# Kernel optimization log

Hardware: AMD Instinct MI355X
Metric: run time of the kernel (lower is better)

Reference implementation:

```python
import jax, jax.numpy as jnp
import numpy as np

D = 1024      # features
C = 768       # context dim
H = 16        # heads
HD = D // H   # head dim = 64
N = 2048      # query tokens
M = 2048      # context tokens
EPS = 1e-12
SCALE = float(np.sqrt(HD))


def layernorm(x, w, b):
    c = x - x.mean(axis=-1, keepdims=True)
    s = (c * c).mean(axis=-1, keepdims=True)
    return c * jax.lax.rsqrt(s + EPS) * w + b


def setup_inputs() -> dict:
    key = jax.random.key(0)
    ks = jax.random.split(key, 10)
    sc = 0.02
    return {
        "x": jax.random.normal(ks[0], (N, D), jnp.float32),
        "ctx": jax.random.normal(ks[1], (M, C), jnp.float32),
        # attention projections (Projection: normal*0.02, zero bias)
        "wq": jax.random.normal(ks[2], (D, D), jnp.float32) * sc,
        "bq": jnp.zeros((D,), jnp.float32),
        "wk": jax.random.normal(ks[3], (C, D), jnp.float32) * sc,
        "bk": jnp.zeros((D,), jnp.float32),
        "wv": jax.random.normal(ks[4], (C, D), jnp.float32) * sc,
        "bv": jnp.zeros((D,), jnp.float32),
        "wo": jax.random.normal(ks[5], (D, D), jnp.float32) * sc,
        "bo": jnp.zeros((D,), jnp.float32),
        # MLP
        "w1": jax.random.normal(ks[6], (D, 4 * D), jnp.float32) * sc,
        "b1": jnp.zeros((4 * D,), jnp.float32),
        "w2": jax.random.normal(ks[7], (4 * D, D), jnp.float32) * sc,
        "b2": jnp.zeros((D,), jnp.float32),
        # layernorms
        "qn_w": jnp.ones((D,), jnp.float32), "qn_b": jnp.zeros((D,), jnp.float32),
        "kvn_w": jnp.ones((C,), jnp.float32), "kvn_b": jnp.zeros((C,), jnp.float32),
        "pn_w": jnp.ones((D,), jnp.float32), "pn_b": jnp.zeros((D,), jnp.float32),
    }


def reference(x, ctx, wq, bq, wk, bk, wv, bv, wo, bo, w1, b1, w2, b2,
              qn_w, qn_b, kvn_w, kvn_b, pn_w, pn_b):
    # pre-norm cross-attention
    xq = layernorm(x, qn_w, qn_b)          # [n, d]
    kv = layernorm(ctx, kvn_w, kvn_b)      # [m, c]
    q = (xq @ wq + bq).reshape(N, H, HD).transpose(1, 0, 2)   # [h, n, hd]
    k = (kv @ wk + bk).reshape(M, H, HD).transpose(1, 0, 2)   # [h, m, hd]
    v = (kv @ wv + bv).reshape(M, H, HD).transpose(1, 0, 2)   # [h, m, hd]
    attn = jax.nn.softmax(jnp.einsum('hnd,hmd->hnm', q, k) / SCALE, axis=-1)
    o = jnp.einsum('hnm,hmd->hnd', attn, v).transpose(1, 0, 2).reshape(N, D)
    x = (o @ wo + bo) + x
    # MLP block
    h = layernorm(x, pn_w, pn_b)
    h = jax.nn.gelu(h @ w1 + b1) @ w2 + b2
    return h + x
```

## Files before the change

### kernel.cpp

```cpp
#include <hip/hip_runtime.h>

typedef __bf16 bf16;
typedef __bf16 bf16x4 __attribute__((ext_vector_type(4)));
typedef __bf16 bf16x8 __attribute__((ext_vector_type(8)));
typedef float f32x4 __attribute__((ext_vector_type(4)));

#define N_TOK 2048
#define M_TOK 2048
#define DIM 1024
#define CDIM 768
#define DFF 4096

static __device__ __forceinline__ void async16(const void* g, void* l) {
  __builtin_amdgcn_global_load_lds((const __attribute__((address_space(1))) void*)g,
                                   (__attribute__((address_space(3))) void*)l, 16, 0, 0);
}

__global__ __launch_bounds__(256) void detect_kernel(const void* x, int* flag) {
  __shared__ int cnt;
  if (threadIdx.x == 0) cnt = 0;
  __syncthreads();
  const unsigned* w = (const unsigned*)x;
  int ok = 0;
  for (int i = threadIdx.x; i < 512; i += 256) {
    unsigned lo = w[i] & 0xFFFFu;
    float f = __uint_as_float(lo << 16);
    if (lo == 0u || (fabsf(f) > 1e-3f && fabsf(f) < 1e3f)) ok++;
  }
  atomicAdd(&cnt, ok);
  __syncthreads();
  if (threadIdx.x == 0) *flag = (cnt >= 256) ? 1 : 0;
}

struct ConvArgs {
  const void* src[12];
  bf16* dst[12];
  int n[12];
};
__global__ __launch_bounds__(256) void conv_small_kernel(ConvArgs a, const int* flag) {
  const bool isbf = (*flag != 0);
  const int b = blockIdx.x;
  const void* in = a.src[b];
  bf16* out = a.dst[b];
  const int n = a.n[b];
  for (int i = threadIdx.x; i < n; i += 256)
    out[i] = isbf ? ((const bf16*)in)[i] : (bf16)((const float*)in)[i];
}

struct TmArgs {
  const void* src[4];
  bf16* dst[4];
  int r0[4], Rcnt[4], c0[4], Cfull[4], gx[4], gy[4];
  int force_bf;
};
__global__ __launch_bounds__(256) void tmulti_kernel(TmArgs a, const int* flag) {
  const int z = blockIdx.z;
  if ((int)blockIdx.x >= a.gx[z] || (int)blockIdx.y >= a.gy[z]) return;
  __shared__ bf16 t[32][33];
  const bool isbf = a.force_bf || (*flag != 0);
  const void* in = a.src[z];
  bf16* out = a.dst[z];
  const int Rcnt = a.Rcnt[z], Cfull = a.Cfull[z];
  const int cb = blockIdx.x * 32, rb = blockIdx.y * 32;
  const int tx = threadIdx.x & 31, ty = threadIdx.x >> 5;
#pragma unroll
  for (int i = 0; i < 4; i++) {
    const size_t r = (size_t)(a.r0[z] + rb + ty + i * 8);
    const size_t c = (size_t)(a.c0[z] + cb + tx);
    float v = isbf ? (float)((const bf16*)in)[r * Cfull + c]
                   : ((const float*)in)[r * Cfull + c];
    t[ty + i * 8][tx] = (bf16)v;
  }
  __syncthreads();
#pragma unroll
  for (int i = 0; i < 4; i++)
    out[(size_t)(cb + ty + i * 8) * Rcnt + rb + tx] = t[tx][ty + i * 8];
}

__global__ __launch_bounds__(256) void ln_pair_kernel(
    const void* __restrict__ x0, const bf16* w0, const bf16* b0, bf16* o0,
    const void* __restrict__ x1, const bf16* w1, const bf16* b1, bf16* o1,
    const int* flag) {
  const bool isbf = (*flag != 0);
  const int cols = (blockIdx.y == 0) ? DIM : CDIM;
  const void* x = (blockIdx.y == 0) ? x0 : x1;
  const bf16* w = (blockIdx.y == 0) ? w0 : w1;
  const bf16* b = (blockIdx.y == 0) ? b0 : b1;
  bf16* outp = (blockIdx.y == 0) ? o0 : o1;
  const int row = blockIdx.x;
  const bf16* xr_b = (const bf16*)x + (size_t)row * cols;
  const float* xr_f = (const float*)x + (size_t)row * cols;
  bf16* orow = outp + (size_t)row * cols;
  float s = 0.f, ss = 0.f;
  for (int c = threadIdx.x; c < cols; c += 256) {
    float v = isbf ? (float)xr_b[c] : xr_f[c];
    s += v; ss += v * v;
  }
  for (int d = 1; d < 64; d <<= 1) { s += __shfl_xor(s, d, 64); ss += __shfl_xor(ss, d, 64); }
  __shared__ float sh[8];
  const int wv = threadIdx.x >> 6, lane = threadIdx.x & 63;
  if (lane == 0) { sh[wv] = s; sh[4 + wv] = ss; }
  __syncthreads();
  s = sh[0] + sh[1] + sh[2] + sh[3];
  ss = sh[4] + sh[5] + sh[6] + sh[7];
  const float mean = s / cols;
  float var = ss / cols - mean * mean;
  var = fmaxf(var, 0.f);
  const float r = rsqrtf(var + 1e-12f);
  for (int c = threadIdx.x; c < cols; c += 256) {
    float v = isbf ? (float)xr_b[c] : xr_f[c];
    orow[c] = (bf16)((v - mean) * r * (float)w[c] + (float)b[c]);
  }
}

__global__ __launch_bounds__(256) void ln_kernel(
    const bf16* __restrict__ x, const bf16* __restrict__ w, const bf16* __restrict__ b,
    bf16* __restrict__ out, int cols) {
  const int row = blockIdx.x;
  const bf16* xr = x + (size_t)row * cols;
  bf16* orow = out + (size_t)row * cols;
  float s = 0.f, ss = 0.f;
  for (int c = threadIdx.x; c < cols; c += 256) {
    float v = (float)xr[c];
    s += v; ss += v * v;
  }
  for (int d = 1; d < 64; d <<= 1) { s += __shfl_xor(s, d, 64); ss += __shfl_xor(ss, d, 64); }
  __shared__ float sh[8];
  const int wv = threadIdx.x >> 6, lane = threadIdx.x & 63;
  if (lane == 0) { sh[wv] = s; sh[4 + wv] = ss; }
  __syncthreads();
  s = sh[0] + sh[1] + sh[2] + sh[3];
  ss = sh[4] + sh[5] + sh[6] + sh[7];
  const float mean = s / cols;
  float var = ss / cols - mean * mean;
  var = fmaxf(var, 0.f);
  const float r = rsqrtf(var + 1e-12f);
  for (int c = threadIdx.x; c < cols; c += 256) {
    float v = (float)xr[c];
    orow[c] = (bf16)((v - mean) * r * (float)w[c] + (float)b[c]);
  }
}

__device__ __forceinline__ float gelu_f(float x) {
  float u = 0.7978845608028654f * (x + 0.044715f * x * x * x);
  return 0.5f * x * (1.f + tanhf(u));
}

template <int EPI>
__global__ __launch_bounds__(256) void gemm64(
    const bf16* __restrict__ A, const bf16* __restrict__ Bt,
    const bf16* __restrict__ bias, const void* __restrict__ resid,
    void* __restrict__ Cout, int K, int ldc, const int* flag) {
  __shared__ __align__(16) bf16 As[64 * 32];
  __shared__ __align__(16) bf16 Bs[64 * 32];
  const int tid = threadIdx.x;
  const int lane = tid & 63, wv = tid >> 6;
  const int lq = lane >> 4, lm = lane & 15;
  const int row0 = blockIdx.y * 64, col0 = blockIdx.x * 64;
  const int wr = (wv >> 1) * 32, wc = (wv & 1) * 32;

  f32x4 acc[2][2] = {};
  const int r_a = wv * 16 + (lane >> 2);
  const int kc = (lane & 3) * 8;

  for (int k0 = 0; k0 < K; k0 += 32) {
    __syncthreads();
    async16(A + (size_t)(row0 + r_a) * K + k0 + kc, As + wv * 512);
    async16(Bt + (size_t)(col0 + r_a) * K + k0 + kc, Bs + wv * 512);
    __syncthreads();
    bf16x8 af[2], bfv[2];
#pragma unroll
    for (int t = 0; t < 2; t++) af[t] = *(const bf16x8*)&As[(wr + t * 16 + lm) * 32 + lq * 8];
#pragma unroll
    for (int t = 0; t < 2; t++) bfv[t] = *(const bf16x8*)&Bs[(wc + t * 16 + lm) * 32 + lq * 8];
#pragma unroll
    for (int i = 0; i < 2; i++)
#pragma unroll
      for (int j = 0; j < 2; j++)
        acc[i][j] = __builtin_amdgcn_mfma_f32_16x16x32_bf16(af[i], bfv[j], acc[i][j], 0, 0, 0);
  }

  const bool isbf = (*flag != 0);
#pragma unroll
  for (int i = 0; i < 2; i++) {
    const int rb = row0 + wr + i * 16 + lq * 4;
#pragma unroll
    for (int j = 0; j < 2; j++) {
      const int c = col0 + wc + j * 16 + lm;
      const float bv = (EPI != 5) ? (float)bias[c] : 0.f;
#pragma unroll
      for (int rg = 0; rg < 4; rg++) {
        const size_t idx = (size_t)(rb + rg) * ldc + c;
        float v = acc[i][j][rg] + bv;
        if (EPI == 1)
          v += isbf ? (float)((const bf16*)resid)[idx] : ((const float*)resid)[idx];
        if (EPI == 2) v = gelu_f(v);
        if (EPI == 4) v += (float)((const bf16*)resid)[idx];
        if (EPI == 5)
          v += isbf ? (float)((bf16*)Cout)[idx] : ((float*)Cout)[idx];
        if (EPI == 4 || EPI == 5) {
          if (isbf) ((bf16*)Cout)[idx] = (bf16)v;
          else      ((float*)Cout)[idx] = v;
        } else {
          ((bf16*)Cout)[idx] = (bf16)v;
        }
      }
    }
  }
}

struct QkvArgs {
  const bf16* A[3];
  const bf16* Bt[3];
  const bf16* bias[3];
  bf16* C[3];
  int K[3];
};
__global__ __launch_bounds__(256) void gemm64_qkv(QkvArgs a) {
  const int z = blockIdx.z;
  const bf16* A = a.A[z];
  const bf16* Bt = a.Bt[z];
  const int K = a.K[z];
  __shared__ __align__(16) bf16 As[64 * 32];
  __shared__ __align__(16) bf16 Bs[64 * 32];
  const int tid = threadIdx.x;
  const int lane = tid & 63, wv = tid >> 6;
  const int lq = lane >> 4, lm = lane & 15;
  const int row0 = blockIdx.y * 64, col0 = blockIdx.x * 64;
  const int wr = (wv >> 1) * 32, wc = (wv & 1) * 32;

  f32x4 acc[2][2] = {};
  const int r_a = wv * 16 + (lane >> 2);
  const int kc = (lane & 3) * 8;

  for (int k0 = 0; k0 < K; k0 += 32) {
    __syncthreads();
    async16(A + (size_t)(row0 + r_a) * K + k0 + kc, As + wv * 512);
    async16(Bt + (size_t)(col0 + r_a) * K + k0 + kc, Bs + wv * 512);
    __syncthreads();
    bf16x8 af[2], bfv[2];
#pragma unroll
    for (int t = 0; t < 2; t++) af[t] = *(const bf16x8*)&As[(wr + t * 16 + lm) * 32 + lq * 8];
#pragma unroll
    for (int t = 0; t < 2; t++) bfv[t] = *(const bf16x8*)&Bs[(wc + t * 16 + lm) * 32 + lq * 8];
#pragma unroll
    for (int i = 0; i < 2; i++)
#pragma unroll
      for (int j = 0; j < 2; j++)
        acc[i][j] = __builtin_amdgcn_mfma_f32_16x16x32_bf16(af[i], bfv[j], acc[i][j], 0, 0, 0);
  }

  const bf16* bias = a.bias[z];
  bf16* C = a.C[z];
#pragma unroll
  for (int i = 0; i < 2; i++) {
    const int rb = row0 + wr + i * 16 + lq * 4;
#pragma unroll
    for (int j = 0; j < 2; j++) {
      const int c = col0 + wc + j * 16 + lm;
      const float bv = (float)bias[c];
#pragma unroll
      for (int rg = 0; rg < 4; rg++)
        C[(size_t)(rb + rg) * DIM + c] = (bf16)(acc[i][j][rg] + bv);
    }
  }
}

#define KS_STR 72
#define VS_STR 136
__global__ __launch_bounds__(256) void attn_kernel(
    const bf16* __restrict__ q, const bf16* __restrict__ k,
    const bf16* __restrict__ vT, bf16* __restrict__ o) {
  __shared__ __align__(16) bf16 Ks[128 * KS_STR];
  __shared__ __align__(16) bf16 Vs[64 * VS_STR];
  __shared__ __align__(16) bf16 Ps[64 * VS_STR];
  const int tid = threadIdx.x, lane = tid & 63, wv = tid >> 6;
  const int lq = lane >> 4, lm = lane & 15;
  const int h = blockIdx.y;
  const int n0 = blockIdx.x * 64;

  bf16x8 qf[2];
#pragma unroll
  for (int f = 0; f < 2; f++)
    qf[f] = *(const bf16x8*)&q[(size_t)(n0 + wv * 16 + lm) * DIM + h * 64 + f * 32 + lq * 8];

  f32x4 oacc[4] = {};
  float lsum = 0.f;
  const float sc = 0.125f * 1.4426950408889634f;

  for (int m0 = 0; m0 < M_TOK; m0 += 128) {
    __syncthreads();
#pragma unroll
    for (int it = 0; it < 4; it++) {
      const int e = tid * 8 + it * 2048;
      const int r = e >> 6, c = e & 63;
      *(bf16x8*)&Ks[r * KS_STR + c] =
          *(const bf16x8*)&k[(size_t)(m0 + r) * DIM + h * 64 + c];
    }
#pragma unroll
    for (int it = 0; it < 4; it++) {
      const int e = tid * 8 + it * 2048;
      const int r = e >> 7, c = e & 127;
      *(bf16x8*)&Vs[r * VS_STR + c] =
          *(const bf16x8*)&vT[(size_t)(h * 64 + r) * M_TOK + m0 + c];
    }
    __syncthreads();

#pragma unroll
    for (int j = 0; j < 8; j++) {
      bf16x8 kf0 = *(const bf16x8*)&Ks[(j * 16 + lm) * KS_STR + lq * 8];
      bf16x8 kf1 = *(const bf16x8*)&Ks[(j * 16 + lm) * KS_STR + 32 + lq * 8];
      f32x4 z = {};
      z = __builtin_amdgcn_mfma_f32_16x16x32_bf16(kf0, qf[0], z, 0, 0, 0);
      z = __builtin_amdgcn_mfma_f32_16x16x32_bf16(kf1, qf[1], z, 0, 0, 0);
      bf16x4 pw;
#pragma unroll
      for (int rg = 0; rg < 4; rg++) {
        const float pv = exp2f(z[rg] * sc);
        lsum += pv;
        pw[rg] = (bf16)pv;
      }
      *(bf16x4*)&Ps[(wv * 16 + lm) * VS_STR + j * 16 + lq * 4] = pw;
    }

#pragma unroll
    for (int kk = 0; kk < 4; kk++) {
      bf16x8 pf = *(const bf16x8*)&Ps[(wv * 16 + lm) * VS_STR + kk * 32 + lq * 8];
#pragma unroll
      for (int dt = 0; dt < 4; dt++) {
        bf16x8 vf = *(const bf16x8*)&Vs[(dt * 16 + lm) * VS_STR + kk * 32 + lq * 8];
        oacc[dt] = __builtin_amdgcn_mfma_f32_16x16x32_bf16(vf, pf, oacc[dt], 0, 0, 0);
      }
    }
  }

  lsum += __shfl_xor(lsum, 16, 64);
  lsum += __shfl_xor(lsum, 32, 64);
  const float rinv = 1.f / lsum;

  const int rn = n0 + wv * 16 + lm;
#pragma unroll
  for (int dt = 0; dt < 4; dt++) {
    bf16x4 ow;
#pragma unroll
    for (int rg = 0; rg < 4; rg++) ow[rg] = (bf16)(oacc[dt][rg] * rinv);
    *(bf16x4*)&o[(size_t)rn * DIM + h * 64 + dt * 16 + lq * 4] = ow;
  }
}

extern "C" void kernel_launch(void* const* d_in, const int* in_sizes, int n_in,
                              void* d_out, int out_size, void* d_ws, size_t ws_size,
                              hipStream_t stream) {
  const void* x_r     = d_in[0];
  const void* ctx_r   = d_in[1];
  const void* wq_r    = d_in[2];
  const void* bq_r    = d_in[3];
  const void* wk_r    = d_in[4];
  const void* bk_r    = d_in[5];
  const void* wv_r    = d_in[6];
  const void* bv_r    = d_in[7];
  const void* wo_r    = d_in[8];
  const void* bo_r    = d_in[9];
  const void* w1_r    = d_in[10];
  const void* b1_r    = d_in[11];
  const void* w2_r    = d_in[12];
  const void* b2_r    = d_in[13];
  const void* qnw_r   = d_in[14];
  const void* qnb_r   = d_in[15];
  const void* kvnw_r  = d_in[16];
  const void* kvnb_r  = d_in[17];
  const void* pnw_r   = d_in[18];
  const void* pnb_r   = d_in[19];

  bf16* p = (bf16*)d_ws;
  const size_t MEG = 1024 * 1024;
  bf16* qm  = p;             bf16* hln = qm;
  bf16* km  = p + 2 * MEG;   bf16* xat = km;
  bf16* wC  = p + 4 * MEG;
  bf16* xq  = p + 8 * MEG;   bf16* om  = xq;
  bf16* vm  = p + 10 * MEG;  bf16* h1h = vm;
  bf16* kvn = p + 12 * MEG;  bf16* vTb = kvn;
  bf16* SM  = p + 14 * MEG;
  int* flag = (int*)(p + 14 * MEG + 16384);

  bf16* wqT = wC;
  bf16* wkT = wC + 1 * MEG;
  bf16* wvT = wC + 1 * MEG + 786432;
  bf16* woT = wC + 2 * MEG + 524288;
  bf16* w1Th = wC;
  bf16* w2Th = wC + 2 * MEG;

  bf16* bqc = SM, *bkc = SM + 1024, *bvc = SM + 2048, *boc = SM + 3072;
  bf16* b1c = SM + 4096, *b2c = SM + 8192;
  bf16* qnw = SM + 9216, *qnb = SM + 10240;
  bf16* kvnw = SM + 11264, *kvnb = SM + 12032;
  bf16* pnw = SM + 12800, *pnb = SM + 13824;

  detect_kernel<<<1, 256, 0, stream>>>(x_r, flag);
  ConvArgs ca;
  ca.src[0] = bq_r;   ca.dst[0] = bqc;  ca.n[0] = DIM;
  ca.src[1] = bk_r;   ca.dst[1] = bkc;  ca.n[1] = DIM;
  ca.src[2] = bv_r;   ca.dst[2] = bvc;  ca.n[2] = DIM;
  ca.src[3] = bo_r;   ca.dst[3] = boc;  ca.n[3] = DIM;
  ca.src[4] = b1_r;   ca.dst[4] = b1c;  ca.n[4] = DFF;
  ca.src[5] = b2_r;   ca.dst[5] = b2c;  ca.n[5] = DIM;
  ca.src[6] = qnw_r;  ca.dst[6] = qnw;  ca.n[6] = DIM;
  ca.src[7] = qnb_r;  ca.dst[7] = qnb;  ca.n[7] = DIM;
  ca.src[8] = kvnw_r; ca.dst[8] = kvnw; ca.n[8] = CDIM;
  ca.src[9] = kvnb_r; ca.dst[9] = kvnb; ca.n[9] = CDIM;
  ca.src[10] = pnw_r; ca.dst[10] = pnw; ca.n[10] = DIM;
  ca.src[11] = pnb_r; ca.dst[11] = pnb; ca.n[11] = DIM;
  conv_small_kernel<<<12, 256, 0, stream>>>(ca, flag);

  ln_pair_kernel<<<dim3(2048, 2), 256, 0, stream>>>(x_r, qnw, qnb, xq,
                                                    ctx_r, kvnw, kvnb, kvn, flag);

  {
    TmArgs ta;
    ta.force_bf = 0;
    ta.src[0] = wq_r; ta.dst[0] = wqT; ta.r0[0] = 0; ta.Rcnt[0] = DIM;
    ta.c0[0] = 0; ta.Cfull[0] = DIM; ta.gx[0] = 32; ta.gy[0] = 32;
    ta.src[1] = wk_r; ta.dst[1] = wkT; ta.r0[1] = 0; ta.Rcnt[1] = CDIM;
    ta.c0[1] = 0; ta.Cfull[1] = DIM; ta.gx[1] = 32; ta.gy[1] = 24;
    ta.src[2] = wv_r; ta.dst[2] = wvT; ta.r0[2] = 0; ta.Rcnt[2] = CDIM;
    ta.c0[2] = 0; ta.Cfull[2] = DIM; ta.gx[2] = 32; ta.gy[2] = 24;
    ta.src[3] = wo_r; ta.dst[3] = woT; ta.r0[3] = 0; ta.Rcnt[3] = DIM;
    ta.c0[3] = 0; ta.Cfull[3] = DIM; ta.gx[3] = 32; ta.gy[3] = 32;
    tmulti_kernel<<<dim3(32, 32, 4), 256, 0, stream>>>(ta, flag);
  }

  {
    QkvArgs qa;
    qa.A[0] = xq;  qa.Bt[0] = wqT; qa.bias[0] = bqc; qa.C[0] = qm; qa.K[0] = DIM;
    qa.A[1] = kvn; qa.Bt[1] = wkT; qa.bias[1] = bkc; qa.C[1] = km; qa.K[1] = CDIM;
    qa.A[2] = kvn; qa.Bt[2] = wvT; qa.bias[2] = bvc; qa.C[2] = vm; qa.K[2] = CDIM;
    gemm64_qkv<<<dim3(16, 32, 3), 256, 0, stream>>>(qa);
  }

  {
    TmArgs ta;
    ta.force_bf = 1;
    ta.src[0] = vm; ta.dst[0] = vTb; ta.r0[0] = 0; ta.Rcnt[0] = M_TOK;
    ta.c0[0] = 0; ta.Cfull[0] = DIM; ta.gx[0] = 32; ta.gy[0] = 64;
    tmulti_kernel<<<dim3(32, 64, 1), 256, 0, stream>>>(ta, flag);
  }

  attn_kernel<<<dim3(32, 16), 256, 0, stream>>>(qm, km, vTb, om);

  gemm64<1><<<dim3(16, 32), 256, 0, stream>>>(om, woT, boc, x_r, xat, DIM, DIM, flag);

  ln_kernel<<<N_TOK, 256, 0, stream>>>(xat, pnw, pnb, hln, DIM);

  for (int hh = 0; hh < 2; hh++) {
    TmArgs ta;
    ta.force_bf = 0;
    ta.src[0] = w1_r; ta.dst[0] = w1Th; ta.r0[0] = 0; ta.Rcnt[0] = DIM;
    ta.c0[0] = hh * 2048; ta.Cfull[0] = DFF; ta.gx[0] = 64; ta.gy[0] = 32;
    ta.src[1] = w2_r; ta.dst[1] = w2Th; ta.r0[1] = hh * 2048; ta.Rcnt[1] = 2048;
    ta.c0[1] = 0; ta.Cfull[1] = DIM; ta.gx[1] = 32; ta.gy[1] = 64;
    ta.src[2] = ta.src[0]; ta.dst[2] = ta.dst[0]; ta.r0[2] = 0; ta.Rcnt[2] = 32;
    ta.c0[2] = 0; ta.Cfull[2] = DIM; ta.gx[2] = 0; ta.gy[2] = 0;
    ta.src[3] = ta.src[0]; ta.dst[3] = ta.dst[0]; ta.r0[3] = 0; ta.Rcnt[3] = 32;
    ta.c0[3] = 0; ta.Cfull[3] = DIM; ta.gx[3] = 0; ta.gy[3] = 0;
    tmulti_kernel<<<dim3(64, 64, 2), 256, 0, stream>>>(ta, flag);

    gemm64<2><<<dim3(32, 32), 256, 0, stream>>>(hln, w1Th, b1c + hh * 2048, nullptr,
                                                h1h, DIM, 2048, flag);
    if (hh == 0)
      gemm64<4><<<dim3(16, 32), 256, 0, stream>>>(h1h, w2Th, b2c, xat, d_out,
                                                  2048, DIM, flag);
    else
      gemm64<5><<<dim3(16, 32), 256, 0, stream>>>(h1h, w2Th, b2c, nullptr, d_out,
                                                  2048, DIM, flag);
  }
}
```

Before: 393.7 us.

## Compute V transposed directly in QKV GEMM, deepen K-step, reuse attention LDS

The V projection now produces V^T directly by swapping operands (wvT as A, kvn as B) with a per-row bias and ldc=M_TOK. This removes the separate transpose kernel launch and the round trip through memory it needed. The GEMMs now load two 32-wide K slabs per barrier pair, halving the synchronisation count. The attention kernel reuses the K staging buffer for P, adding a barrier to cut LDS use. The qkv grid is enlarged, so some blocks exit immediately.

```diff
diff --git a/kernel.cpp b/kernel.cpp
--- a/kernel.cpp
+++ b/kernel.cpp
@@ -151,8 +151,8 @@
     const bf16* __restrict__ A, const bf16* __restrict__ Bt,
     const bf16* __restrict__ bias, const void* __restrict__ resid,
     void* __restrict__ Cout, int K, int ldc, const int* flag) {
-  __shared__ __align__(16) bf16 As[64 * 32];
-  __shared__ __align__(16) bf16 Bs[64 * 32];
+  __shared__ __align__(16) bf16 As[2][64 * 32];
+  __shared__ __align__(16) bf16 Bs[2][64 * 32];
   const int tid = threadIdx.x;
   const int lane = tid & 63, wv = tid >> 6;
   const int lq = lane >> 4, lm = lane & 15;
@@ -163,21 +163,29 @@
   const int r_a = wv * 16 + (lane >> 2);
   const int kc = (lane & 3) * 8;
 
-  for (int k0 = 0; k0 < K; k0 += 32) {
-    __syncthreads();
-    async16(A + (size_t)(row0 + r_a) * K + k0 + kc, As + wv * 512);
-    async16(Bt + (size_t)(col0 + r_a) * K + k0 + kc, Bs + wv * 512);
-    __syncthreads();
-    bf16x8 af[2], bfv[2];
-#pragma unroll
-    for (int t = 0; t < 2; t++) af[t] = *(const bf16x8*)&As[(wr + t * 16 + lm) * 32 + lq * 8];
-#pragma unroll
-    for (int t = 0; t < 2; t++) bfv[t] = *(const bf16x8*)&Bs[(wc + t * 16 + lm) * 32 + lq * 8];
-#pragma unroll
-    for (int i = 0; i < 2; i++)
-#pragma unroll
-      for (int j = 0; j < 2; j++)
-        acc[i][j] = __builtin_amdgcn_mfma_f32_16x16x32_bf16(af[i], bfv[j], acc[i][j], 0, 0, 0);
+  for (int k0 = 0; k0 < K; k0 += 64) {
+    __syncthreads();
+#pragma unroll
+    for (int b = 0; b < 2; b++) {
+      async16(A + (size_t)(row0 + r_a) * K + k0 + b * 32 + kc, As[b] + wv * 512);
+      async16(Bt + (size_t)(col0 + r_a) * K + k0 + b * 32 + kc, Bs[b] + wv * 512);
+    }
+    __syncthreads();
+#pragma unroll
+    for (int b = 0; b < 2; b++) {
+      bf16x8 af[2], bfv[2];
+#pragma unroll
+      for (int t = 0; t < 2; t++)
+        af[t] = *(const bf16x8*)&As[b][(wr + t * 16 + lm) * 32 + lq * 8];
+#pragma unroll
+      for (int t = 0; t < 2; t++)
+        bfv[t] = *(const bf16x8*)&Bs[b][(wc + t * 16 + lm) * 32 + lq * 8];
+#pragma unroll
+      for (int i = 0; i < 2; i++)
+#pragma unroll
+        for (int j = 0; j < 2; j++)
+          acc[i][j] = __builtin_amdgcn_mfma_f32_16x16x32_bf16(af[i], bfv[j], acc[i][j], 0, 0, 0);
+    }
   }
 
   const bool isbf = (*flag != 0);
@@ -214,15 +222,16 @@
   const bf16* Bt[3];
   const bf16* bias[3];
   bf16* C[3];
-  int K[3];
+  int K[3], ldc[3], gx[3], gy[3], brow[3];
 };
 __global__ __launch_bounds__(256) void gemm64_qkv(QkvArgs a) {
   const int z = blockIdx.z;
+  if ((int)blockIdx.x >= a.gx[z] || (int)blockIdx.y >= a.gy[z]) return;
   const bf16* A = a.A[z];
   const bf16* Bt = a.Bt[z];
   const int K = a.K[z];
-  __shared__ __align__(16) bf16 As[64 * 32];
-  __shared__ __align__(16) bf16 Bs[64 * 32];
+  __shared__ __align__(16) bf16 As[2][64 * 32];
+  __shared__ __align__(16) bf16 Bs[2][64 * 32];
   const int tid = threadIdx.x;
   const int lane = tid & 63, wv = tid >> 6;
   const int lq = lane >> 4, lm = lane & 15;
@@ -233,35 +242,47 @@
   const int r_a = wv * 16 + (lane >> 2);
   const int kc = (lane & 3) * 8;
 
-  for (int k0 = 0; k0 < K; k0 += 32) {
-    __syncthreads();
-    async16(A + (size_t)(row0 + r_a) * K + k0 + kc, As + wv * 512);
-    async16(Bt + (size_t)(col0 + r_a) * K + k0 + kc, Bs + wv * 512);
-    __syncthreads();
-    bf16x8 af[2], bfv[2];
-#pragma unroll
-    for (int t = 0; t < 2; t++) af[t] = *(const bf16x8*)&As[(wr + t * 16 + lm) * 32 + lq * 8];
-#pragma unroll
-    for (int t = 0; t < 2; t++) bfv[t] = *(const bf16x8*)&Bs[(wc + t * 16 + lm) * 32 + lq * 8];
-#pragma unroll
-    for (int i = 0; i < 2; i++)
-#pragma unroll
-      for (int j = 0; j < 2; j++)
-        acc[i][j] = __builtin_amdgcn_mfma_f32_16x16x32_bf16(af[i], bfv[j], acc[i][j], 0, 0, 0);
+  for (int k0 = 0; k0 < K; k0 += 64) {
+    __syncthreads();
+#pragma unroll
+    for (int b = 0; b < 2; b++) {
+      async16(A + (size_t)(row0 + r_a) * K + k0 + b * 32 + kc, As[b] + wv * 512);
+      async16(Bt + (size_t)(col0 + r_a) * K + k0 + b * 32 + kc, Bs[b] + wv * 512);
+    }
+    __syncthreads();
+#pragma unroll
+    for (int b = 0; b < 2; b++) {
+      bf16x8 af[2], bfv[2];
+#pragma unroll
+      for (int t = 0; t < 2; t++)
+        af[t] = *(const bf16x8*)&As[b][(wr + t * 16 + lm) * 32 + lq * 8];
+#pragma unroll
+      for (int t = 0; t < 2; t++)
+        bfv[t] = *(const bf16x8*)&Bs[b][(wc + t * 16 + lm) * 32 + lq * 8];
+#pragma unroll
+      for (int i = 0; i < 2; i++)
+#pragma unroll
+        for (int j = 0; j < 2; j++)
+          acc[i][j] = __builtin_amdgcn_mfma_f32_16x16x32_bf16(af[i], bfv[j], acc[i][j], 0, 0, 0);
+    }
   }
 
   const bf16* bias = a.bias[z];
   bf16* C = a.C[z];
+  const int ldc = a.ldc[z];
+  const bool brow = a.brow[z] != 0;
 #pragma unroll
   for (int i = 0; i < 2; i++) {
     const int rb = row0 + wr + i * 16 + lq * 4;
 #pragma unroll
     for (int j = 0; j < 2; j++) {
       const int c = col0 + wc + j * 16 + lm;
-      const float bv = (float)bias[c];
-#pragma unroll
-      for (int rg = 0; rg < 4; rg++)
-        C[(size_t)(rb + rg) * DIM + c] = (bf16)(acc[i][j][rg] + bv);
+      const float bcol = brow ? 0.f : (float)bias[c];
+#pragma unroll
+      for (int rg = 0; rg < 4; rg++) {
+        const float bv = brow ? (float)bias[rb + rg] : bcol;
+        C[(size_t)(rb + rg) * ldc + c] = (bf16)(acc[i][j][rg] + bv);
+      }
     }
   }
 }
@@ -271,9 +292,8 @@
 __global__ __launch_bounds__(256) void attn_kernel(
     const bf16* __restrict__ q, const bf16* __restrict__ k,
     const bf16* __restrict__ vT, bf16* __restrict__ o) {
-  __shared__ __align__(16) bf16 Ks[128 * KS_STR];
+  __shared__ __align__(16) bf16 KPs[128 * KS_STR];
   __shared__ __align__(16) bf16 Vs[64 * VS_STR];
-  __shared__ __align__(16) bf16 Ps[64 * VS_STR];
   const int tid = threadIdx.x, lane = tid & 63, wv = tid >> 6;
   const int lq = lane >> 4, lm = lane & 15;
   const int h = blockIdx.y;
@@ -294,7 +314,7 @@
     for (int it = 0; it < 4; it++) {
       const int e = tid * 8 + it * 2048;
       const int r = e >> 6, c = e & 63;
-      *(bf16x8*)&Ks[r * KS_STR + c] =
+      *(bf16x8*)&KPs[r * KS_STR + c] =
           *(const bf16x8*)&k[(size_t)(m0 + r) * DIM + h * 64 + c];
     }
 #pragma unroll
@@ -306,26 +326,32 @@
     }
     __syncthreads();
 
+    f32x4 s[8];
 #pragma unroll
     for (int j = 0; j < 8; j++) {
-      bf16x8 kf0 = *(const bf16x8*)&Ks[(j * 16 + lm) * KS_STR + lq * 8];
-      bf16x8 kf1 = *(const bf16x8*)&Ks[(j * 16 + lm) * KS_STR + 32 + lq * 8];
+      bf16x8 kf0 = *(const bf16x8*)&KPs[(j * 16 + lm) * KS_STR + lq * 8];
+      bf16x8 kf1 = *(const bf16x8*)&KPs[(j * 16 + lm) * KS_STR + 32 + lq * 8];
       f32x4 z = {};
       z = __builtin_amdgcn_mfma_f32_16x16x32_bf16(kf0, qf[0], z, 0, 0, 0);
-      z = __builtin_amdgcn_mfma_f32_16x16x32_bf16(kf1, qf[1], z, 0, 0, 0);
+      s[j] = __builtin_amdgcn_mfma_f32_16x16x32_bf16(kf1, qf[1], z, 0, 0, 0);
+    }
+    __syncthreads();
+
+#pragma unroll
+    for (int j = 0; j < 8; j++) {
       bf16x4 pw;
 #pragma unroll
       for (int rg = 0; rg < 4; rg++) {
-        const float pv = exp2f(z[rg] * sc);
+        const float pv = exp2f(s[j][rg] * sc);
         lsum += pv;
         pw[rg] = (bf16)pv;
       }
-      *(bf16x4*)&Ps[(wv * 16 + lm) * VS_STR + j * 16 + lq * 4] = pw;
+      *(bf16x4*)&KPs[(wv * 16 + lm) * VS_STR + j * 16 + lq * 4] = pw;
     }
 
 #pragma unroll
     for (int kk = 0; kk < 4; kk++) {
-      bf16x8 pf = *(const bf16x8*)&Ps[(wv * 16 + lm) * VS_STR + kk * 32 + lq * 8];
+      bf16x8 pf = *(const bf16x8*)&KPs[(wv * 16 + lm) * VS_STR + kk * 32 + lq * 8];
 #pragma unroll
       for (int dt = 0; dt < 4; dt++) {
         bf16x8 vf = *(const bf16x8*)&Vs[(dt * 16 + lm) * VS_STR + kk * 32 + lq * 8];
@@ -378,8 +404,9 @@
   bf16* km  = p + 2 * MEG;   bf16* xat = km;
   bf16* wC  = p + 4 * MEG;
   bf16* xq  = p + 8 * MEG;   bf16* om  = xq;
-  bf16* vm  = p + 10 * MEG;  bf16* h1h = vm;
-  bf16* kvn = p + 12 * MEG;  bf16* vTb = kvn;
+  bf16* h1h = p + 10 * MEG;
+  bf16* kvn = p + 12 * MEG;
+  bf16* vTb = p + 10 * MEG;
   bf16* SM  = p + 14 * MEG;
   int* flag = (int*)(p + 14 * MEG + 16384);
 
@@ -431,18 +458,13 @@
 
   {
     QkvArgs qa;
-    qa.A[0] = xq;  qa.Bt[0] = wqT; qa.bias[0] = bqc; qa.C[0] = qm; qa.K[0] = DIM;
-    qa.A[1] = kvn; qa.Bt[1] = wkT; qa.bias[1] = bkc; qa.C[1] = km; qa.K[1] = CDIM;
-    qa.A[2] = kvn; qa.Bt[2] = wvT; qa.bias[2] = bvc; qa.C[2] = vm; qa.K[2] = CDIM;
-    gemm64_qkv<<<dim3(16, 32, 3), 256, 0, stream>>>(qa);
-  }
-
-  {
-    TmArgs ta;
-    ta.force_bf = 1;
-    ta.src[0] = vm; ta.dst[0] = vTb; ta.r0[0] = 0; ta.Rcnt[0] = M_TOK;
-    ta.c0[0] = 0; ta.Cfull[0] = DIM; ta.gx[0] = 32; ta.gy[0] = 64;
-    tmulti_kernel<<<dim3(32, 64, 1), 256, 0, stream>>>(ta, flag);
+    qa.A[0] = xq;  qa.Bt[0] = wqT; qa.bias[0] = bqc; qa.C[0] = qm;
+    qa.K[0] = DIM;  qa.ldc[0] = DIM;   qa.gx[0] = 16; qa.gy[0] = 32; qa.brow[0] = 0;
+    qa.A[1] = kvn; qa.Bt[1] = wkT; qa.bias[1] = bkc; qa.C[1] = km;
+    qa.K[1] = CDIM; qa.ldc[1] = DIM;   qa.gx[1] = 16; qa.gy[1] = 32; qa.brow[1] = 0;
+    qa.A[2] = wvT; qa.Bt[2] = kvn; qa.bias[2] = bvc; qa.C[2] = vTb;
+    qa.K[2] = CDIM; qa.ldc[2] = M_TOK; qa.gx[2] = 32; qa.gy[2] = 16; qa.brow[2] = 1;
+    gemm64_qkv<<<dim3(32, 32, 3), 256, 0, stream>>>(qa);
   }
 
   attn_kernel<<<dim3(32, 16), 256, 0, stream>>>(qm, km, vTb, om);
```

Result: no change. 387.4 us (-1.6%).
